# Optimization experiments

Hardware: AMD Instinct MI355X
Metric: run time of the kernel (lower is better)

Reference implementation:

```python
import jax, jax.numpy as jnp
import numpy as np

N = 100000       # nodes
E = 1600000      # edges (before self-loops)
D = 128          # input feature dim
H = 128          # hidden width (both hidden GATConv layers)
OUT = 128        # out_channel
NEG_SLOPE = 0.2  # PyG GATConv default


def setup_inputs() -> dict:
    key = jax.random.key(0)
    ks = jax.random.split(key, 16)
    x = jax.random.normal(ks[0], (N, D), dtype=jnp.float32)
    edge_index = jax.random.randint(ks[1], (2, E), 0, N, dtype=jnp.int64)

    def layer_params(k, din, dout):
        k1, k2, k3 = jax.random.split(k, 3)
        W = jax.random.normal(k1, (din, dout), dtype=jnp.float32) * (1.0 / np.sqrt(din))
        a_src = jax.random.normal(k2, (dout,), dtype=jnp.float32) * 0.1
        a_dst = jax.random.normal(k3, (dout,), dtype=jnp.float32) * 0.1
        b = jnp.zeros((dout,), dtype=jnp.float32)
        return W, a_src, a_dst, b

    W0, as0, ad0, b0 = layer_params(ks[2], D, H)
    W1, as1, ad1, b1 = layer_params(ks[3], H, H)
    W2, as2, ad2, b2 = layer_params(ks[4], H, OUT)
    return {
        "x": x, "edge_index": edge_index,
        "W0": W0, "as0": as0, "ad0": ad0, "b0": b0,
        "W1": W1, "as1": as1, "ad1": ad1, "b1": b1,
        "W2": W2, "as2": as2, "ad2": ad2, "b2": b2,
    }


def _gat_conv(x, src, dst, W, a_src, a_dst, b):
    """PyG GATConv, heads=1: gather -> edge attention softmax (per dst) -> scatter-add."""
    h = x @ W                                  # [N, C]
    alpha_s = h @ a_src                        # [N] per-source scalar
    alpha_d = h @ a_dst                        # [N] per-dest scalar
    e = jax.nn.leaky_relu(alpha_s[src] + alpha_d[dst], NEG_SLOPE)  # [Etot]
    # numerically stable softmax over edges grouped by destination node
    m = jax.ops.segment_max(e, dst, num_segments=N)
    ex = jnp.exp(e - m[dst])
    denom = jax.ops.segment_sum(ex, dst, num_segments=N)
    w = ex / denom[dst]                        # [Etot] attention coeffs
    out = jax.ops.segment_sum(h[src] * w[:, None], dst, num_segments=N)
    return out + b


def reference(x, edge_index, W0, as0, ad0, b0, W1, as1, ad1, b1, W2, as2, ad2, b2):
    # GATConv adds self-loops by default; edge_index[0]=source j, [1]=target i
    loops = jnp.arange(N, dtype=edge_index.dtype)
    src = jnp.concatenate([edge_index[0], loops])
    dst = jnp.concatenate([edge_index[1], loops])

    h = jax.nn.relu(_gat_conv(x, src, dst, W0, as0, ad0, b0))
    h = jax.nn.relu(_gat_conv(h, src, dst, W1, as1, ad1, b1))
    return _gat_conv(h, src, dst, W2, as2, ad2, b2)
```

## Files before the change

kernel.cpp:

```cpp
#include <hip/hip_runtime.h>

#define NN 100000
#define EE 1600000
#define NB 391
#define CHUNK 2048

typedef __attribute__((ext_vector_type(8))) short bf16x8;
typedef __attribute__((ext_vector_type(4))) float f32x4;

static __device__ __forceinline__ unsigned short f2bf(float f) {
  unsigned u = __float_as_uint(f);
  u += 0x7fffu + ((u >> 16) & 1u);
  return (unsigned short)(u >> 16);
}
static __device__ __forceinline__ float bf2f(unsigned short s) {
  return __uint_as_float(((unsigned)s) << 16);
}


__global__ void zero_aux(int* __restrict__ bcnt, int* __restrict__ bfill) {
  int i = blockIdx.x * 256 + threadIdx.x;
  if (i < NB * 16) { bcnt[i] = 0; bfill[i] = 0; }
}

__launch_bounds__(256)
__global__ void bucket_hist(const int* __restrict__ dst, int* __restrict__ bcnt) {
  __shared__ int hist[NB];
  int tid = threadIdx.x;
  for (int i = tid; i < NB; i += 256) hist[i] = 0;
  __syncthreads();
  int e0 = blockIdx.x * CHUNK;
  int n = min(CHUNK, EE - e0);
  for (int i = tid; i < n; i += 256) atomicAdd(&hist[dst[e0 + i] >> 8], 1);
  __syncthreads();
  for (int i = tid; i < NB; i += 256) {
    int c = hist[i];
    if (c) atomicAdd(&bcnt[i * 16], c);
  }
}

__launch_bounds__(256)
__global__ void bucket_scan(const int* __restrict__ bcnt, int* __restrict__ bOffC,
                            int* __restrict__ offsets) {
  __shared__ int wpart[4];
  __shared__ int carryS;
  int tid = threadIdx.x, lane = tid & 63, w = tid >> 6;
  if (tid == 0) carryS = 0;
  __syncthreads();
  for (int base = 0; base < NB; base += 256) {
    int i = base + tid;
    int v = (i < NB) ? bcnt[i * 16] : 0;
    int x = v;
    #pragma unroll
    for (int d = 1; d < 64; d <<= 1) { int y = __shfl_up(x, d); if (lane >= d) x += y; }
    if (lane == 63) wpart[w] = x;
    __syncthreads();
    int wbase = 0;
    #pragma unroll
    for (int k = 0; k < 3; ++k) if (k < w) wbase += wpart[k];
    int tot = wpart[0] + wpart[1] + wpart[2] + wpart[3];
    int carry = carryS;
    if (i < NB) bOffC[i] = carry + wbase + x - v;
    __syncthreads();
    if (tid == 0) carryS = carry + tot;
    __syncthreads();
  }
  if (tid == 0) offsets[NN] = EE + NN;
}

__launch_bounds__(256)
__global__ void bucket_scatter(const int* __restrict__ ei, const int* __restrict__ bOffC,
                               int* __restrict__ bfill, long long* __restrict__ pairs) {
  __shared__ int hist[NB];
  __shared__ int lofs[NB];
  __shared__ int resv[NB];
  __shared__ long long stage[CHUNK];
  __shared__ int wpart[4];
  int tid = threadIdx.x, lane = tid & 63, w = tid >> 6;
  int e0 = blockIdx.x * CHUNK;
  int n = min(CHUNK, EE - e0);
  for (int i = tid; i < NB; i += 256) hist[i] = 0;
  __syncthreads();

  int s[8], d[8], lp[8], bk[8];
  #pragma unroll
  for (int q = 0; q < 8; ++q) {
    int i = q * 256 + tid;
    if (i < n) {
      s[q] = ei[e0 + i];
      d[q] = ei[EE + e0 + i];
      bk[q] = d[q] >> 8;
      lp[q] = atomicAdd(&hist[bk[q]], 1);
    }
  }
  __syncthreads();

  int carry = 0;
  for (int base = 0; base < NB; base += 256) {
    int i = base + tid;
    int v = (i < NB) ? hist[i] : 0;
    int x = v;
    #pragma unroll
    for (int dd = 1; dd < 64; dd <<= 1) { int y = __shfl_up(x, dd); if (lane >= dd) x += y; }
    if (lane == 63) wpart[w] = x;
    __syncthreads();
    int wbase = 0;
    #pragma unroll
    for (int k = 0; k < 3; ++k) if (k < w) wbase += wpart[k];
    int tot = wpart[0] + wpart[1] + wpart[2] + wpart[3];
    if (i < NB) lofs[i] = carry + wbase + x - v;
    __syncthreads();
    carry += tot;
  }

  #pragma unroll
  for (int q = 0; q < 8; ++q) {
    int i = q * 256 + tid;
    if (i < n) stage[lofs[bk[q]] + lp[q]] = ((long long)d[q] << 32) | (unsigned)s[q];
  }
  for (int b = tid; b < NB; b += 256) {
    int c = hist[b];
    resv[b] = c ? atomicAdd(&bfill[b * 16], c) : 0;
  }
  __syncthreads();
  for (int i = tid; i < n; i += 256) {
    long long pd = stage[i];
    int dd = (int)(pd >> 32);
    int b = dd >> 8;
    pairs[(size_t)bOffC[b] + resv[b] + (i - lofs[b])] = pd;
  }
}

__launch_bounds__(256)
__global__ void build_csr(const long long* __restrict__ pairs, const int* __restrict__ bOffC,
                          const int* __restrict__ bcnt, int* __restrict__ offsets,
                          int* __restrict__ srcs) {
  __shared__ int deg[256];
  __shared__ int intra[256];
  __shared__ int fil[256];
  __shared__ int wpart[4];
  int b = blockIdx.x, tid = threadIdx.x;
  int n0 = b << 8;
  int nodes = min(256, NN - n0);
  int ecnt = bcnt[b * 16];
  size_t pbase = (size_t)bOffC[b];
  int cbase = bOffC[b] + n0;
  deg[tid] = 0; fil[tid] = 0;
  __syncthreads();
  for (int i = tid; i < ecnt; i += 256) {
    int dd = (int)(pairs[pbase + i] >> 32);
    atomicAdd(&deg[dd - n0], 1);
  }
  __syncthreads();
  int v = (tid < nodes) ? deg[tid] + 1 : 0;
  int lane = tid & 63, w = tid >> 6;
  int x = v;
  #pragma unroll
  for (int dd = 1; dd < 64; dd <<= 1) { int y = __shfl_up(x, dd); if (lane >= dd) x += y; }
  if (lane == 63) wpart[w] = x;
  __syncthreads();
  int wbase = 0;
  #pragma unroll
  for (int k = 0; k < 3; ++k) if (k < w) wbase += wpart[k];
  int excl = wbase + x - v;
  if (tid < nodes) { intra[tid] = excl; offsets[n0 + tid] = cbase + excl; }
  __syncthreads();
  for (int i = tid; i < ecnt; i += 256) {
    long long pd = pairs[pbase + i];
    int dd = (int)(pd >> 32), ss = (int)pd;
    int ln = dd - n0;
    int p = atomicAdd(&fil[ln], 1);
    srcs[cbase + intra[ln] + p] = ss;
  }
  __syncthreads();
  if (tid < nodes) srcs[cbase + intra[tid] + deg[tid]] = n0 + tid;
}


__global__ void prep_w3(const float* __restrict__ Wa, const float* __restrict__ Wb,
                        const float* __restrict__ Wc, short* __restrict__ Whi,
                        short* __restrict__ Wlo) {
  int t = blockIdx.x * 256 + threadIdx.x;
  int L = t >> 11;
  int tt = t & 2047;
  const float* W = (L == 0) ? Wa : (L == 1) ? Wb : Wc;
  int lane = tt & 63, ct = (tt >> 6) & 7, kt = tt >> 9;
  int l4 = lane & 15, grp = lane >> 4;
  int c = ct * 16 + l4;
  int k0 = kt * 32 + grp * 8;
  bf16x8 hi, lo;
  #pragma unroll
  for (int i = 0; i < 8; ++i) {
    float w = W[(k0 + i) * 128 + c];
    unsigned short h = f2bf(w);
    hi[i] = (short)h;
    lo[i] = (short)f2bf(w - bf2f(h));
  }
  size_t off = (size_t)L * 131072 + ((size_t)(kt * 8 + ct) * 64 + lane) * 8;
  *(bf16x8*)&Whi[off] = hi;
  *(bf16x8*)&Wlo[off] = lo;
}


__launch_bounds__(256, 2)
__global__ void transform_mfma(const float* __restrict__ x,
                               const short* __restrict__ Whi, const short* __restrict__ Wlo,
                               const float* __restrict__ a_src, const float* __restrict__ a_dst,
                               unsigned short* __restrict__ hb,
                               float* __restrict__ alphaS, float* __restrict__ alphaD) {
  __shared__ unsigned short lh[4][32][132];
  int tid = threadIdx.x;
  int lane = tid & 63, wid = tid >> 6;
  int l4 = lane & 15, grp = lane >> 4;
  int rbase = blockIdx.x * 128 + wid * 32;

  const float* xr[2];
  #pragma unroll
  for (int rt = 0; rt < 2; ++rt) {
    int R = rbase + rt * 16 + l4;
    xr[rt] = x + (size_t)(R < NN ? R : 0) * 128;
  }

  f32x4 acc[2][8];
  #pragma unroll
  for (int rt = 0; rt < 2; ++rt)
    #pragma unroll
    for (int ct = 0; ct < 8; ++ct) acc[rt][ct] = (f32x4)(0.f);

  #pragma unroll
  for (int kt = 0; kt < 4; ++kt) {
    bf16x8 Ahi[2], Alo[2];
    #pragma unroll
    for (int rt = 0; rt < 2; ++rt) {
      const float* p = xr[rt] + kt * 32 + grp * 8;
      float4 v0 = *(const float4*)p;
      float4 v1 = *(const float4*)(p + 4);
      float f[8] = {v0.x, v0.y, v0.z, v0.w, v1.x, v1.y, v1.z, v1.w};
      #pragma unroll
      for (int i = 0; i < 8; ++i) {
        unsigned short h = f2bf(f[i]);
        Ahi[rt][i] = (short)h;
        Alo[rt][i] = (short)f2bf(f[i] - bf2f(h));
      }
    }
    #pragma unroll
    for (int ct = 0; ct < 8; ++ct) {
      size_t off = ((size_t)(kt * 8 + ct) * 64 + lane) * 8;
      bf16x8 bh = *(const bf16x8*)&Whi[off];
      bf16x8 bl = *(const bf16x8*)&Wlo[off];
      #pragma unroll
      for (int rt = 0; rt < 2; ++rt) {
        acc[rt][ct] = __builtin_amdgcn_mfma_f32_16x16x32_bf16(Ahi[rt], bh, acc[rt][ct], 0, 0, 0);
        acc[rt][ct] = __builtin_amdgcn_mfma_f32_16x16x32_bf16(Ahi[rt], bl, acc[rt][ct], 0, 0, 0);
        acc[rt][ct] = __builtin_amdgcn_mfma_f32_16x16x32_bf16(Alo[rt], bh, acc[rt][ct], 0, 0, 0);
      }
    }
  }

  float asv[8], adv[8];
  #pragma unroll
  for (int ct = 0; ct < 8; ++ct) { asv[ct] = a_src[ct * 16 + l4]; adv[ct] = a_dst[ct * 16 + l4]; }

  #pragma unroll
  for (int rt = 0; rt < 2; ++rt) {
    #pragma unroll
    for (int reg = 0; reg < 4; ++reg) {
      float ps = 0.f, pd = 0.f;
      #pragma unroll
      for (int ct = 0; ct < 8; ++ct) {
        ps = fmaf(acc[rt][ct][reg], asv[ct], ps);
        pd = fmaf(acc[rt][ct][reg], adv[ct], pd);
      }
      #pragma unroll
      for (int mdl = 1; mdl < 16; mdl <<= 1) {
        ps += __shfl_xor(ps, mdl);
        pd += __shfl_xor(pd, mdl);
      }
      int row = rbase + rt * 16 + grp * 4 + reg;
      if (l4 == 0 && row < NN) { alphaS[row] = ps; alphaD[row] = pd; }
    }
    #pragma unroll
    for (int reg = 0; reg < 4; ++reg) {
      int lrow = rt * 16 + grp * 4 + reg;
      #pragma unroll
      for (int ct = 0; ct < 8; ++ct)
        lh[wid][lrow][ct * 16 + l4] = f2bf(acc[rt][ct][reg]);
    }
  }

  #pragma unroll
  for (int it = 0; it < 8; ++it) {
    int lrow = it * 4 + (lane >> 4);
    int chunk = lane & 15;
    int row = rbase + lrow;
    if (row < NN) {
      const unsigned short* p = &lh[wid][lrow][chunk * 8];
      uint4 v = {*(const unsigned*)&p[0] , *(const unsigned*)&p[2],
                 *(const unsigned*)&p[4] , *(const unsigned*)&p[6]};
      *(uint4*)&hb[(size_t)row * 128 + chunk * 8] = v;
    }
  }
}


template<bool RELU>
__launch_bounds__(256)
__global__ void agg_kernel(const unsigned short* __restrict__ hb,
                           const float* __restrict__ alphaS, const float* __restrict__ alphaD,
                           const int* __restrict__ offsets, const int* __restrict__ srcs,
                           const float* __restrict__ bias, float* __restrict__ out) {
  int lane = threadIdx.x & 63;
  int node = (blockIdx.x * 256 + threadIdx.x) >> 6;
  if (node >= NN) return;
  int beg = offsets[node], end = offsets[node + 1];
  float aD = alphaD[node];

  int l4 = lane & 15, grp = lane >> 4;
  float a[8];
  #pragma unroll
  for (int i = 0; i < 8; ++i) a[i] = 0.f;
  float ssum = 0.f;

  for (int j0 = beg; j0 < end; j0 += 64) {
    int j = j0 + lane;
    int cnt = min(64, end - j0);
    int s = 0; float t = 0.f;
    if (j < end) {
      int sv = srcs[j];
      float e = alphaS[sv] + aD;
      e = (e >= 0.f) ? e : 0.2f * e;
      t = __expf(e);
      s = sv;
    }
    ssum += t;
    for (int jj = 0; jj < cnt; jj += 4) {
      int e2 = jj + grp;
      int sv   = __shfl(s, e2);
      float tv = __shfl(t, e2);
      if (tv > 0.f) {
        uint4 hp = *(const uint4*)&hb[(size_t)sv * 128 + l4 * 8];
        a[0] = fmaf(tv, __uint_as_float(hp.x << 16),           a[0]);
        a[1] = fmaf(tv, __uint_as_float(hp.x & 0xffff0000u),   a[1]);
        a[2] = fmaf(tv, __uint_as_float(hp.y << 16),           a[2]);
        a[3] = fmaf(tv, __uint_as_float(hp.y & 0xffff0000u),   a[3]);
        a[4] = fmaf(tv, __uint_as_float(hp.z << 16),           a[4]);
        a[5] = fmaf(tv, __uint_as_float(hp.z & 0xffff0000u),   a[5]);
        a[6] = fmaf(tv, __uint_as_float(hp.w << 16),           a[6]);
        a[7] = fmaf(tv, __uint_as_float(hp.w & 0xffff0000u),   a[7]);
      }
    }
  }
  #pragma unroll
  for (int d2 = 1; d2 < 64; d2 <<= 1) ssum += __shfl_xor(ssum, d2);
  float inv = 1.f / ssum;

  #pragma unroll
  for (int i = 0; i < 8; ++i) {
    a[i] += __shfl_xor(a[i], 16);
    a[i] += __shfl_xor(a[i], 32);
  }
  if (grp == 0) {
    float4 b0 = *(const float4*)&bias[l4 * 8];
    float4 b1 = *(const float4*)&bias[l4 * 8 + 4];
    float4 o0 = {fmaf(a[0], inv, b0.x), fmaf(a[1], inv, b0.y),
                 fmaf(a[2], inv, b0.z), fmaf(a[3], inv, b0.w)};
    float4 o1 = {fmaf(a[4], inv, b1.x), fmaf(a[5], inv, b1.y),
                 fmaf(a[6], inv, b1.z), fmaf(a[7], inv, b1.w)};
    if (RELU) {
      o0.x = fmaxf(o0.x, 0.f); o0.y = fmaxf(o0.y, 0.f);
      o0.z = fmaxf(o0.z, 0.f); o0.w = fmaxf(o0.w, 0.f);
      o1.x = fmaxf(o1.x, 0.f); o1.y = fmaxf(o1.y, 0.f);
      o1.z = fmaxf(o1.z, 0.f); o1.w = fmaxf(o1.w, 0.f);
    }
    *(float4*)&out[(size_t)node * 128 + l4 * 8]     = o0;
    *(float4*)&out[(size_t)node * 128 + l4 * 8 + 4] = o1;
  }
}


extern "C" void kernel_launch(void* const* d_in, const int* in_sizes, int n_in,
                              void* d_out, int out_size, void* d_ws, size_t ws_size,
                              hipStream_t stream) {
  const float* x   = (const float*)d_in[0];
  const int*   ei  = (const int*)d_in[1];
  const float* W0  = (const float*)d_in[2];
  const float* as0 = (const float*)d_in[3];
  const float* ad0 = (const float*)d_in[4];
  const float* b0  = (const float*)d_in[5];
  const float* W1  = (const float*)d_in[6];
  const float* as1 = (const float*)d_in[7];
  const float* ad1 = (const float*)d_in[8];
  const float* b1  = (const float*)d_in[9];
  const float* W2  = (const float*)d_in[10];
  const float* as2 = (const float*)d_in[11];
  const float* ad2 = (const float*)d_in[12];
  const float* b2  = (const float*)d_in[13];
  float* out = (float*)d_out;

  long long* pairs = (long long*)d_ws;
  short* Whi = (short*)(pairs + EE);
  short* Wlo = Whi + 3 * 131072;
  unsigned short* hb = (unsigned short*)(Wlo + 3 * 131072);
  float* alphaS = (float*)(hb + (size_t)NN * 128);
  float* alphaD = alphaS + NN;
  int*   offsets = (int*)(alphaD + NN);
  int*   srcs    = offsets + NN + 1;
  int*   bcnt    = srcs + EE + NN;
  int*   bfill   = bcnt + NB * 16;
  int*   bOffC   = bfill + NB * 16;

  const int cgrid = (EE + CHUNK - 1) / CHUNK;

  prep_w3<<<24, 256, 0, stream>>>(W0, W1, W2, Whi, Wlo);
  zero_aux<<<(NB * 16 + 255) / 256, 256, 0, stream>>>(bcnt, bfill);
  bucket_hist<<<cgrid, 256, 0, stream>>>(ei + EE, bcnt);
  bucket_scan<<<1, 256, 0, stream>>>(bcnt, bOffC, offsets);
  bucket_scatter<<<cgrid, 256, 0, stream>>>(ei, bOffC, bfill, pairs);
  build_csr<<<NB, 256, 0, stream>>>(pairs, bOffC, bcnt, offsets, srcs);

  const int tgrid = (NN + 127) / 128;
  const int agrid = (NN + 3) / 4;

  transform_mfma<<<tgrid, 256, 0, stream>>>(x, Whi, Wlo, as0, ad0, hb, alphaS, alphaD);
  agg_kernel<true><<<agrid, 256, 0, stream>>>(hb, alphaS, alphaD, offsets, srcs, b0, out);

  transform_mfma<<<tgrid, 256, 0, stream>>>(out, Whi + 131072, Wlo + 131072, as1, ad1, hb, alphaS, alphaD);
  agg_kernel<true><<<agrid, 256, 0, stream>>>(hb, alphaS, alphaD, offsets, srcs, b1, out);

  transform_mfma<<<tgrid, 256, 0, stream>>>(out, Whi + 262144, Wlo + 262144, as2, ad2, hb, alphaS, alphaD);
  agg_kernel<false><<<agrid, 256, 0, stream>>>(hb, alphaS, alphaD, offsets, srcs, b2, out);
}
```

Measured before the change: 404.0 us.

## Stage weights in LDS for transform, store directly, and unroll aggregation gathers

```diff
diff --git a/kernel.cpp b/kernel.cpp
--- a/kernel.cpp
+++ b/kernel.cpp
@@ -202,13 +202,14 @@
 }
 
 
-__launch_bounds__(256, 2)
+__launch_bounds__(256)
 __global__ void transform_mfma(const float* __restrict__ x,
                                const short* __restrict__ Whi, const short* __restrict__ Wlo,
                                const float* __restrict__ a_src, const float* __restrict__ a_dst,
                                unsigned short* __restrict__ hb,
                                float* __restrict__ alphaS, float* __restrict__ alphaD) {
-  __shared__ unsigned short lh[4][32][132];
+  __shared__ short WhiS[4096];
+  __shared__ short WloS[4096];
   int tid = threadIdx.x;
   int lane = tid & 63, wid = tid >> 6;
   int l4 = lane & 15, grp = lane >> 4;
@@ -227,7 +228,6 @@
     #pragma unroll
     for (int ct = 0; ct < 8; ++ct) acc[rt][ct] = (f32x4)(0.f);
 
-  #pragma unroll
   for (int kt = 0; kt < 4; ++kt) {
     bf16x8 Ahi[2], Alo[2];
     #pragma unroll
@@ -243,11 +243,19 @@
         Alo[rt][i] = (short)f2bf(f[i] - bf2f(h));
       }
     }
+    __syncthreads();
+    {
+      int base = kt * 4096 + tid * 16;
+      *(bf16x8*)&WhiS[tid * 16]     = *(const bf16x8*)&Whi[base];
+      *(bf16x8*)&WhiS[tid * 16 + 8] = *(const bf16x8*)&Whi[base + 8];
+      *(bf16x8*)&WloS[tid * 16]     = *(const bf16x8*)&Wlo[base];
+      *(bf16x8*)&WloS[tid * 16 + 8] = *(const bf16x8*)&Wlo[base + 8];
+    }
+    __syncthreads();
     #pragma unroll
     for (int ct = 0; ct < 8; ++ct) {
-      size_t off = ((size_t)(kt * 8 + ct) * 64 + lane) * 8;
-      bf16x8 bh = *(const bf16x8*)&Whi[off];
-      bf16x8 bl = *(const bf16x8*)&Wlo[off];
+      bf16x8 bh = *(const bf16x8*)&WhiS[(ct * 64 + lane) * 8];
+      bf16x8 bl = *(const bf16x8*)&WloS[(ct * 64 + lane) * 8];
       #pragma unroll
       for (int rt = 0; rt < 2; ++rt) {
         acc[rt][ct] = __builtin_amdgcn_mfma_f32_16x16x32_bf16(Ahi[rt], bh, acc[rt][ct], 0, 0, 0);
@@ -281,23 +289,12 @@
     }
     #pragma unroll
     for (int reg = 0; reg < 4; ++reg) {
-      int lrow = rt * 16 + grp * 4 + reg;
-      #pragma unroll
-      for (int ct = 0; ct < 8; ++ct)
-        lh[wid][lrow][ct * 16 + l4] = f2bf(acc[rt][ct][reg]);
-    }
-  }
-
-  #pragma unroll
-  for (int it = 0; it < 8; ++it) {
-    int lrow = it * 4 + (lane >> 4);
-    int chunk = lane & 15;
-    int row = rbase + lrow;
-    if (row < NN) {
-      const unsigned short* p = &lh[wid][lrow][chunk * 8];
-      uint4 v = {*(const unsigned*)&p[0] , *(const unsigned*)&p[2],
-                 *(const unsigned*)&p[4] , *(const unsigned*)&p[6]};
-      *(uint4*)&hb[(size_t)row * 128 + chunk * 8] = v;
+      int row = rbase + rt * 16 + grp * 4 + reg;
+      if (row < NN) {
+        #pragma unroll
+        for (int ct = 0; ct < 8; ++ct)
+          hb[(size_t)row * 128 + ct * 16 + l4] = f2bf(acc[rt][ct][reg]);
+      }
     }
   }
 }
@@ -333,21 +330,31 @@
       s = sv;
     }
     ssum += t;
-    for (int jj = 0; jj < cnt; jj += 4) {
-      int e2 = jj + grp;
-      int sv   = __shfl(s, e2);
-      float tv = __shfl(t, e2);
-      if (tv > 0.f) {
-        uint4 hp = *(const uint4*)&hb[(size_t)sv * 128 + l4 * 8];
-        a[0] = fmaf(tv, __uint_as_float(hp.x << 16),           a[0]);
-        a[1] = fmaf(tv, __uint_as_float(hp.x & 0xffff0000u),   a[1]);
-        a[2] = fmaf(tv, __uint_as_float(hp.y << 16),           a[2]);
-        a[3] = fmaf(tv, __uint_as_float(hp.y & 0xffff0000u),   a[3]);
-        a[4] = fmaf(tv, __uint_as_float(hp.z << 16),           a[4]);
-        a[5] = fmaf(tv, __uint_as_float(hp.z & 0xffff0000u),   a[5]);
-        a[6] = fmaf(tv, __uint_as_float(hp.w << 16),           a[6]);
-        a[7] = fmaf(tv, __uint_as_float(hp.w & 0xffff0000u),   a[7]);
-      }
+    for (int jj = 0; jj < cnt; jj += 8) {
+      int eA = jj + grp;
+      int eB = eA + 4;
+      int svA   = __shfl(s, eA);
+      float tA  = __shfl(t, eA);
+      int svB   = __shfl(s, eB);
+      float tB  = __shfl(t, eB);
+      uint4 hA = *(const uint4*)&hb[(size_t)svA * 128 + l4 * 8];
+      uint4 hB = *(const uint4*)&hb[(size_t)svB * 128 + l4 * 8];
+      a[0] = fmaf(tA, __uint_as_float(hA.x << 16),           a[0]);
+      a[1] = fmaf(tA, __uint_as_float(hA.x & 0xffff0000u),   a[1]);
+      a[2] = fmaf(tA, __uint_as_float(hA.y << 16),           a[2]);
+      a[3] = fmaf(tA, __uint_as_float(hA.y & 0xffff0000u),   a[3]);
+      a[4] = fmaf(tA, __uint_as_float(hA.z << 16),           a[4]);
+      a[5] = fmaf(tA, __uint_as_float(hA.z & 0xffff0000u),   a[5]);
+      a[6] = fmaf(tA, __uint_as_float(hA.w << 16),           a[6]);
+      a[7] = fmaf(tA, __uint_as_float(hA.w & 0xffff0000u),   a[7]);
+      a[0] = fmaf(tB, __uint_as_float(hB.x << 16),           a[0]);
+      a[1] = fmaf(tB, __uint_as_float(hB.x & 0xffff0000u),   a[1]);
+      a[2] = fmaf(tB, __uint_as_float(hB.y << 16),           a[2]);
+      a[3] = fmaf(tB, __uint_as_float(hB.y & 0xffff0000u),   a[3]);
+      a[4] = fmaf(tB, __uint_as_float(hB.z << 16),           a[4]);
+      a[5] = fmaf(tB, __uint_as_float(hB.z & 0xffff0000u),   a[5]);
+      a[6] = fmaf(tB, __uint_as_float(hB.w << 16),           a[6]);
+      a[7] = fmaf(tB, __uint_as_float(hB.w & 0xffff0000u),   a[7]);
     }
   }
   #pragma unroll
```

New measurement: 369.9 us. -8.4%, faster.
